# Kernel tuning notes

Hardware: AMD Instinct MI355X
Metric: run time of the kernel (lower is better)

Reference implementation:

```python
import jax, jax.numpy as jnp
import numpy as np
import math

NHEAD = 8
OUT = 64
EF = 64
IN = 256
NTYPES = 5
NH = 50000
NT = 100000
E = 800000
NEG_SLOPE = 0.2

def _uniform(key, shape, fan):
    # matches reset(): uniform(-stdv, stdv), stdv = sqrt(6/(fan_in+fan_out)) over last two dims
    stdv = math.sqrt(6.0 / (shape[-2] + shape[-1]))
    return jax.random.uniform(key, shape, jnp.float32, -stdv, stdv)

def setup_inputs() -> dict:
    key = jax.random.key(0)
    ks = jax.random.split(key, 12)
    head_feature = jax.random.normal(ks[0], (NH, IN), jnp.float32)
    tail_feature = jax.random.normal(ks[1], (NT, IN), jnp.float32)
    head_ind = jax.random.randint(ks[2], (E,), 0, NH)
    tail_ind = jax.random.randint(ks[3], (E,), 0, NT)
    tmp_edge = jax.random.randint(ks[4], (E,), 0, NTYPES)
    edge_emb = _uniform(ks[5], (NTYPES, EF), None)
    W = _uniform(ks[6], (IN, OUT * NHEAD), None)
    W_e = _uniform(ks[7], (EF, EF * NHEAD), None)
    a_l = _uniform(ks[8], (1, NHEAD, OUT), None)
    a_r = _uniform(ks[9], (1, NHEAD, OUT), None)
    a_e = _uniform(ks[10], (1, NHEAD, EF), None)
    return {"head_feature": head_feature, "tail_feature": tail_feature,
            "head_ind": head_ind, "tail_ind": tail_ind, "tmp_edge": tmp_edge,
            "edge_emb": edge_emb, "W": W, "W_e": W_e,
            "a_l": a_l, "a_r": a_r, "a_e": a_e}

def reference(head_feature, tail_feature, head_ind, tail_ind, tmp_edge,
              edge_emb, W, W_e, a_l, a_r, a_e):
    n_head_nodes = head_feature.shape[0]
    # projections (dropout is identity in eval)
    h_head = (head_feature @ W).reshape(-1, NHEAD, OUT)   # [NH, H, D]
    h_tail = (tail_feature @ W).reshape(-1, NHEAD, OUT)   # [NT, H, D]
    e = (edge_emb @ W_e).reshape(-1, NHEAD, EF)           # [T, H, EF]
    # per-edge attention logits, all heads at once: [E, H]
    h_l = jnp.sum(a_l * h_head, axis=-1)[head_ind]
    h_r = jnp.sum(a_r * h_tail, axis=-1)[tail_ind]
    h_e = jnp.sum(a_e * e, axis=-1)[tmp_edge]
    att = jax.nn.leaky_relu(h_l + h_r + h_e, NEG_SLOPE)
    # sparse (per-destination-row) softmax, vectorized over heads
    seg_max = jax.ops.segment_max(att, head_ind, num_segments=n_head_nodes)
    att = jnp.exp(att - seg_max[head_ind])
    denom = jax.ops.segment_sum(att, head_ind, num_segments=n_head_nodes)
    att = att / denom[head_ind]                           # [E, H]
    # weighted aggregation per head (small fixed loop over heads)
    outs = [jax.ops.segment_sum(att[:, n:n + 1] * h_tail[tail_ind, n, :],
                                head_ind, num_segments=n_head_nodes)
            for n in range(NHEAD)]
    out = jnp.stack(outs, axis=1).reshape(n_head_nodes, -1)  # [NH, H*D]
    return out, att
```

## Files before the change

### kernel.cpp

```cpp
#include <hip/hip_runtime.h>

#define NH 50000
#define NT 100000
#define NE 800000
#define MPAD 100096

typedef __attribute__((ext_vector_type(8))) short bf16x8;
typedef __attribute__((ext_vector_type(4))) float f32x4;

__device__ __forceinline__ unsigned short f2bf(float f){
  unsigned int u = __float_as_uint(f);
  u += 0x7FFFu + ((u >> 16) & 1u);
  return (unsigned short)(u >> 16);
}

__device__ __forceinline__ void fma8(float* acc, float w, uint4 pk){
  acc[0] += w*__uint_as_float(pk.x<<16); acc[1] += w*__uint_as_float(pk.x&0xFFFF0000u);
  acc[2] += w*__uint_as_float(pk.y<<16); acc[3] += w*__uint_as_float(pk.y&0xFFFF0000u);
  acc[4] += w*__uint_as_float(pk.z<<16); acc[5] += w*__uint_as_float(pk.z&0xFFFF0000u);
  acc[6] += w*__uint_as_float(pk.w<<16); acc[7] += w*__uint_as_float(pk.w&0xFFFF0000u);
}

__global__ void k_prep(const float* __restrict__ W, const float* __restrict__ W_e,
                       const float* __restrict__ edge_emb,
                       const float* __restrict__ a_l, const float* __restrict__ a_r,
                       const float* __restrict__ a_e,
                       unsigned short* __restrict__ wlr_t,
                       float* __restrict__ h_e){
  __shared__ float s_al[512], s_ar[512], s_ae[512], s_wef[512];
  int t = threadIdx.x;
  for (int i=t;i<512;i+=256){ s_al[i]=a_l[i]; s_ar[i]=a_r[i]; s_ae[i]=a_e[i]; }
  __syncthreads();
  { int k = t;
    for (int h=0;h<8;h++){
      float accl=0.f, accr=0.f;
      for (int d=0; d<64; d++){
        float w = W[k*512 + h*64 + d];
        accl += w*s_al[h*64+d];
        accr += w*s_ar[h*64+d];
      }
      wlr_t[h*256 + k]     = f2bf(accl);
      wlr_t[(8+h)*256 + k] = f2bf(accr);
    }
  }
  if (t<64){
    for (int h=0;h<8;h++){
      float acc=0.f;
      for (int f=0; f<64; f++) acc += W_e[t*512 + h*64 + f]*s_ae[h*64+f];
      s_wef[t*8+h]=acc;
    }
  }
  __syncthreads();
  if (t<40){
    int ty=t>>3, h=t&7;
    float acc=0.f;
    for (int k2=0;k2<64;k2++) acc += edge_emb[ty*64+k2]*s_wef[k2*8+h];
    h_e[t]=acc;
  }
}

__global__ void k_wt(const float* __restrict__ W, unsigned short* __restrict__ Wt){
  int n = blockIdx.x, k = threadIdx.x;
  Wt[n*256+k] = f2bf(W[k*512+n]);
}

__global__ __launch_bounds__(256) void k_hl(const float* __restrict__ head_f,
      const unsigned short* __restrict__ wlr_t, float* __restrict__ h_l){
  __shared__ unsigned short As[256*64];
  __shared__ unsigned short Bs[16*256];
  int t = threadIdx.x;
  int wave = t>>6, lane = t&63;
  int lr = lane&15, lq = lane>>4;
  long r0 = (long)blockIdx.x*256;

#pragma unroll
  for (int i=0;i<2;i++){
    int q = i*256 + t;
    int c = q>>5, un = q&31;
    float4 v = *(const float4*)(wlr_t + c*256 + un*8);
    int u = un ^ (c&7);
    *(float4*)((char*)Bs + c*512 + u*16) = v;
  }

  f32x4 acc[4];
#pragma unroll
  for (int mf=0;mf<4;mf++) acc[mf]=(f32x4){0.f,0.f,0.f,0.f};

  for (int kt=0; kt<4; kt++){
    __syncthreads();
#pragma unroll
    for (int i=0;i<16;i++){
      int q = i*256+t;
      int row = q>>4, cg = q&15;
      long gr = r0 + row;
      float4 v = make_float4(0.f,0.f,0.f,0.f);
      if (gr < NH) v = *(const float4*)(head_f + gr*256 + kt*64 + cg*4);
      int u = (cg>>1) ^ (row&7);
      ushort4 sv;
      sv.x=f2bf(v.x); sv.y=f2bf(v.y); sv.z=f2bf(v.z); sv.w=f2bf(v.w);
      *(ushort4*)((char*)As + row*128 + u*16 + (cg&1)*8) = sv;
    }
    __syncthreads();
#pragma unroll
    for (int ks=0;ks<2;ks++){
      int un = kt*8 + ks*4 + lq;
      int cu = un ^ (lr&7);
      bf16x8 bfr = *(const bf16x8*)((const char*)Bs + lr*512 + cu*16);
#pragma unroll
      for (int mf=0;mf<4;mf++){
        int r = wave*64 + mf*16 + lr;
        int u = (ks*4+lq) ^ (r&7);
        bf16x8 afr = *(const bf16x8*)((const char*)As + r*128 + u*16);
        acc[mf] = __builtin_amdgcn_mfma_f32_16x16x32_bf16(afr, bfr, acc[mf], 0,0,0);
      }
    }
  }
#pragma unroll
  for (int mf=0;mf<4;mf++)
#pragma unroll
    for (int j=0;j<4;j++){
      long grow = r0 + wave*64 + mf*16 + lq*4 + j;
      if (grow < NH && lr < 8) h_l[grow*8+lr] = acc[mf][j];
    }
}

__global__ __launch_bounds__(256) void k_gemm(const float* __restrict__ Aref,
      const unsigned short* __restrict__ Wt, const float* __restrict__ a_r_g,
      unsigned short* __restrict__ Cout, float* __restrict__ h_r){
  __shared__ unsigned short As[128*64];
  __shared__ unsigned short Bs[128*64];
  int t = threadIdx.x;
  int m0 = blockIdx.x*128;
  int n0 = blockIdx.y*128;
  int wave = t>>6, lane = t&63;
  int wm = (wave>>1)*64, wn = (wave&1)*64;
  int lr = lane & 15, lq = lane >> 4;

  f32x4 acc[4][4];
#pragma unroll
  for (int mf=0;mf<4;mf++)
#pragma unroll
    for (int nf=0;nf<4;nf++) acc[mf][nf] = (f32x4){0.f,0.f,0.f,0.f};

  for (int kt=0; kt<4; kt++){
#pragma unroll
    for (int i=0;i<8;i++){
      int q = i*256 + t;
      int row = q>>4;
      int cg  = q&15;
      int grow = m0 + row;
      float4 v = make_float4(0.f,0.f,0.f,0.f);
      if (grow < NT) v = *(const float4*)(Aref + (size_t)grow*256 + kt*64 + cg*4);
      int u  = (cg>>1) ^ (row&7);
      ushort4 sv;
      sv.x=f2bf(v.x); sv.y=f2bf(v.y); sv.z=f2bf(v.z); sv.w=f2bf(v.w);
      *(ushort4*)((char*)As + row*128 + u*16 + (cg&1)*8) = sv;
    }
#pragma unroll
    for (int i=0;i<4;i++){
      int q = i*256 + t;
      int row = q>>3;
      int un  = q&7;
      float4 v = *(const float4*)(Wt + (size_t)(n0+row)*256 + kt*64 + un*8);
      int u = un ^ (row&7);
      *(float4*)((char*)Bs + row*128 + u*16) = v;
    }
    __syncthreads();

    bf16x8 af[2][4], bfr[2][4];
#pragma unroll
    for (int ks=0;ks<2;ks++)
#pragma unroll
      for (int mf=0;mf<4;mf++){
        int r = wm + mf*16 + lr;
        int u = (ks*4 + lq) ^ (r&7);
        af[ks][mf] = *(const bf16x8*)((const char*)As + r*128 + u*16);
      }
#pragma unroll
    for (int ks=0;ks<2;ks++)
#pragma unroll
      for (int nf=0;nf<4;nf++){
        int c = wn + nf*16 + lr;
        int u = (ks*4 + lq) ^ (c&7);
        bfr[ks][nf] = *(const bf16x8*)((const char*)Bs + c*128 + u*16);
      }
#pragma unroll
    for (int ks=0;ks<2;ks++)
#pragma unroll
      for (int mf=0;mf<4;mf++)
#pragma unroll
        for (int nf=0;nf<4;nf++)
          acc[mf][nf] = __builtin_amdgcn_mfma_f32_16x16x32_bf16(af[ks][mf], bfr[ks][nf], acc[mf][nf], 0,0,0);
    __syncthreads();
  }
#pragma unroll
  for (int mf=0;mf<4;mf++)
#pragma unroll
    for (int nf=0;nf<4;nf++){
      int gr = m0 + wm + mf*16 + lq*4;
      int gc = n0 + wn + nf*16 + lr;
#pragma unroll
      for (int j=0;j<4;j++)
        Cout[(size_t)(gr+j)*512 + gc] = f2bf(acc[mf][nf][j]);
    }
  {
    int h = (n0 + wn) >> 6;
    float w[4];
#pragma unroll
    for (int nf=0;nf<4;nf++) w[nf] = a_r_g[h*64 + nf*16 + lr];
#pragma unroll
    for (int mf=0;mf<4;mf++)
#pragma unroll
      for (int j=0;j<4;j++){
        float s = acc[mf][0][j]*w[0] + acc[mf][1][j]*w[1]
                + acc[mf][2][j]*w[2] + acc[mf][3][j]*w[3];
        s += __shfl_xor(s, 1); s += __shfl_xor(s, 2);
        s += __shfl_xor(s, 4); s += __shfl_xor(s, 8);
        int gr = m0 + wm + mf*16 + lq*4 + j;
        if (lr == 0 && gr < NT) h_r[(size_t)gr*8 + h] = s;
      }
  }
}

__global__ void k_hist(const int* __restrict__ head_ind, int* __restrict__ cnt){
  int e = blockIdx.x*256 + threadIdx.x;
  atomicAdd(&cnt[head_ind[e]], 1);
}

__global__ void k_scan1(const int* __restrict__ cnt, int* __restrict__ bsum){
  __shared__ int s[256];
  int b=blockIdx.x, t=threadIdx.x, g=b*256+t;
  s[t] = (g<NH)? cnt[g] : 0;
  __syncthreads();
  for (int off=128; off>0; off>>=1){ if (t<off) s[t]+=s[t+off]; __syncthreads(); }
  if (t==0) bsum[b]=s[0];
}
__global__ void k_scan2(int* __restrict__ bsum, int nb){
  __shared__ int s[256];
  int t=threadIdx.x;
  int v = (t<nb)? bsum[t] : 0;
  s[t]=v; __syncthreads();
  for (int off=1; off<256; off<<=1){
    int u = (t>=off)? s[t-off] : 0; __syncthreads();
    s[t]+=u; __syncthreads();
  }
  if (t<nb) bsum[t] = s[t]-v;
}
__global__ void k_scan3(const int* __restrict__ cnt, const int* __restrict__ bsum,
                        int* __restrict__ offs, int* __restrict__ cur){
  __shared__ int s[256];
  int b=blockIdx.x, t=threadIdx.x, g=b*256+t;
  int v=(g<NH)? cnt[g] : 0;
  s[t]=v; __syncthreads();
  for (int off=1; off<256; off<<=1){
    int u=(t>=off)? s[t-off] : 0; __syncthreads();
    s[t]+=u; __syncthreads();
  }
  int excl = s[t]-v + bsum[b];
  if (g<NH){
    offs[g]=excl; cur[g]=excl;
    if (g==NH-1) offs[NH]=excl+v;
  }
}

__global__ void k_logit2(const int* __restrict__ head_ind, const int* __restrict__ tail_ind,
                         const int* __restrict__ tmp_edge,
                         const float* __restrict__ h_l, const float* __restrict__ h_r,
                         const float* __restrict__ h_e,
                         int* __restrict__ cur,
                         float* __restrict__ att_csr,
                         int* __restrict__ edge_of, int* __restrict__ tail_s){
  int g = blockIdx.x*256 + threadIdx.x;
  int e = g>>3, h = g&7, l = threadIdx.x&63;
  int hd = head_ind[e], tl = tail_ind[e], ty = tmp_edge[e];
  float v = h_l[hd*8+h] + h_r[(size_t)tl*8+h] + h_e[ty*8+h];
  v = v > 0.f ? v : 0.2f*v;
  int p = 0;
  if (h==0) p = atomicAdd(&cur[hd], 1);
  p = __shfl(p, l & ~7);
  att_csr[p*8+h] = v;
  if (h==0){ edge_of[p]=e; tail_s[p]=tl; }
}

__global__ __launch_bounds__(256) void k_agg3(const int* __restrict__ offs,
      const int* __restrict__ edge_of, const int* __restrict__ tail_s,
      const float* __restrict__ att_csr,
      const unsigned short* __restrict__ h_tail,
      float* __restrict__ att, float* __restrict__ out){
  int t = threadIdx.x;
  int l = t & 63;
  int i = blockIdx.x*4 + (t>>6);
  int h = l & 7, hq = l >> 3;
  int s0 = offs[i];
  int deg = offs[i+1] - s0;

  float m = -1e30f;
  for (int q = hq; q < deg; q += 8) m = fmaxf(m, att_csr[(s0+q)*8 + h]);
  m = fmaxf(m, __shfl_xor(m, 8));
  m = fmaxf(m, __shfl_xor(m, 16));
  m = fmaxf(m, __shfl_xor(m, 32));
  float sum = 0.f;
  for (int q = hq; q < deg; q += 8) sum += __expf(att_csr[(s0+q)*8 + h] - m);
  sum += __shfl_xor(sum, 8); sum += __shfl_xor(sum, 16); sum += __shfl_xor(sum, 32);
  float r = (deg > 0) ? 1.f/sum : 0.f;

  float mh = __shfl(m, hq), rh = __shfl(r, hq);
  bool wlane = (l & 7) == 0;
  float acc[8];
#pragma unroll
  for (int c=0;c<8;c++) acc[c]=0.f;
  int j = 0;
  for (; j+4 <= deg; j += 4){
    int p0=s0+j, p1=p0+1, p2=p0+2, p3=p0+3;
    int t0=tail_s[p0], t1=tail_s[p1], t2=tail_s[p2], t3=tail_s[p3];
    float a0=att_csr[p0*8+hq], a1=att_csr[p1*8+hq];
    float a2=att_csr[p2*8+hq], a3=att_csr[p3*8+hq];
    uint4 r0 = *(const uint4*)(h_tail + (size_t)t0*512 + l*8);
    uint4 r1 = *(const uint4*)(h_tail + (size_t)t1*512 + l*8);
    uint4 r2 = *(const uint4*)(h_tail + (size_t)t2*512 + l*8);
    uint4 r3 = *(const uint4*)(h_tail + (size_t)t3*512 + l*8);
    float w0=__expf(a0-mh)*rh, w1=__expf(a1-mh)*rh;
    float w2=__expf(a2-mh)*rh, w3=__expf(a3-mh)*rh;
    if (wlane){
      __builtin_nontemporal_store(w0, &att[(size_t)edge_of[p0]*8 + hq]);
      __builtin_nontemporal_store(w1, &att[(size_t)edge_of[p1]*8 + hq]);
      __builtin_nontemporal_store(w2, &att[(size_t)edge_of[p2]*8 + hq]);
      __builtin_nontemporal_store(w3, &att[(size_t)edge_of[p3]*8 + hq]);
    }
    fma8(acc, w0, r0);
    fma8(acc, w1, r1);
    fma8(acc, w2, r2);
    fma8(acc, w3, r3);
  }
  for (; j < deg; j++){
    int p0 = s0+j;
    int t0 = tail_s[p0];
    float a0 = att_csr[p0*8 + hq];
    uint4 r0 = *(const uint4*)(h_tail + (size_t)t0*512 + l*8);
    float w0 = __expf(a0 - mh) * rh;
    if (wlane) __builtin_nontemporal_store(w0, &att[(size_t)edge_of[p0]*8 + hq]);
    fma8(acc, w0, r0);
  }
  float* o = out + (size_t)i*512 + l*8;
  f32x4 v0 = {acc[0],acc[1],acc[2],acc[3]};
  f32x4 v1 = {acc[4],acc[5],acc[6],acc[7]};
  __builtin_nontemporal_store(v0, (f32x4*)o);
  __builtin_nontemporal_store(v1, (f32x4*)(o+4));
}

extern "C" void kernel_launch(void* const* d_in, const int* in_sizes, int n_in,
                              void* d_out, int out_size, void* d_ws, size_t ws_size,
                              hipStream_t stream) {
  const float* head_f   = (const float*)d_in[0];
  const float* tail_f   = (const float*)d_in[1];
  const int*   head_ind = (const int*)d_in[2];
  const int*   tail_ind = (const int*)d_in[3];
  const int*   tmp_edge = (const int*)d_in[4];
  const float* edge_emb = (const float*)d_in[5];
  const float* W        = (const float*)d_in[6];
  const float* W_e      = (const float*)d_in[7];
  const float* a_l      = (const float*)d_in[8];
  const float* a_r      = (const float*)d_in[9];
  const float* a_e      = (const float*)d_in[10];

  float* out = (float*)d_out;
  float* att = out + (size_t)NH*512;

  char* ws = (char*)d_ws;
  auto alloc = [&](size_t bytes)->char*{ char* p = ws; ws += (bytes+511)&~(size_t)511; return p; };
  unsigned short* Wt    = (unsigned short*)alloc((size_t)512*256*2);
  unsigned short* wlr_t = (unsigned short*)alloc((size_t)16*256*2);
  float* h_e            = (float*)alloc(512);
  float* h_l            = (float*)alloc((size_t)NH*8*4);
  float* h_r            = (float*)alloc((size_t)NT*8*4);
  unsigned short* h_tail= (unsigned short*)alloc((size_t)MPAD*512*2);
  int* cnt              = (int*)alloc((size_t)NH*4);
  int* offs             = (int*)alloc((size_t)(NH+1)*4);
  int* cur              = (int*)alloc((size_t)NH*4);
  int* bsum             = (int*)alloc(1024);
  int* edge_of          = (int*)alloc((size_t)NE*4);
  int* tail_s           = (int*)alloc((size_t)NE*4);
  float* att_csr        = (float*)alloc((size_t)NE*8*4);

  hipMemsetAsync(cnt, 0, (size_t)NH*4, stream);
  k_prep<<<1,256,0,stream>>>(W, W_e, edge_emb, a_l, a_r, a_e, wlr_t, h_e);
  k_wt<<<512,256,0,stream>>>(W, Wt);
  k_hl<<<(NH+255)/256,256,0,stream>>>(head_f, wlr_t, h_l);
  k_gemm<<<dim3(MPAD/128,4),256,0,stream>>>(tail_f, Wt, a_r, h_tail, h_r);
  k_hist<<<NE/256,256,0,stream>>>(head_ind, cnt);
  k_scan1<<<196,256,0,stream>>>(cnt, bsum);
  k_scan2<<<1,256,0,stream>>>(bsum, 196);
  k_scan3<<<196,256,0,stream>>>(cnt, bsum, offs, cur);
  k_logit2<<<NE*8/256,256,0,stream>>>(head_ind, tail_ind, tmp_edge, h_l, h_r, h_e,
                                      cur, att_csr, edge_of, tail_s);
  k_agg3<<<NH/4,256,0,stream>>>(offs, edge_of, tail_s, att_csr, h_tail, att, out);
}
```

Measured before the change: 465.6 us.

## Pre-convert tail features to bf16 and double-buffer GEMM with direct global-to-LDS loads

Adds a separate pass that converts tail_feature to bf16 into the output buffer, used as scratch before it is overwritten. The tail projection GEMM now stages A and B tiles straight into LDS with global_load_lds into two buffers, prefetching the next K tile while computing the current one. It also remaps block IDs so each XCD works on a contiguous range of tiles. The aim is to remove in-loop fp32-to-bf16 conversion and register staging and to overlap loads with MFMA, at the cost of an extra conversion kernel's memory traffic.

```diff
diff --git a/kernel.cpp b/kernel.cpp
--- a/kernel.cpp
+++ b/kernel.cpp
@@ -7,6 +7,7 @@
 
 typedef __attribute__((ext_vector_type(8))) short bf16x8;
 typedef __attribute__((ext_vector_type(4))) float f32x4;
+typedef __attribute__((ext_vector_type(8))) unsigned short u16x8;
 
 __device__ __forceinline__ unsigned short f2bf(float f){
   unsigned int u = __float_as_uint(f);
@@ -19,6 +20,12 @@
   acc[2] += w*__uint_as_float(pk.y<<16); acc[3] += w*__uint_as_float(pk.y&0xFFFF0000u);
   acc[4] += w*__uint_as_float(pk.z<<16); acc[5] += w*__uint_as_float(pk.z&0xFFFF0000u);
   acc[6] += w*__uint_as_float(pk.w<<16); acc[7] += w*__uint_as_float(pk.w&0xFFFF0000u);
+}
+
+__device__ __forceinline__ void gl2lds16(const unsigned short* g, unsigned short* l){
+  __builtin_amdgcn_global_load_lds(
+      (const __attribute__((address_space(1))) void*)g,
+      (__attribute__((address_space(3))) void*)l, 16, 0, 0);
 }
 
 __global__ void k_prep(const float* __restrict__ W, const float* __restrict__ W_e,
@@ -64,6 +71,18 @@
   Wt[n*256+k] = f2bf(W[k*512+n]);
 }
 
+__global__ __launch_bounds__(256) void k_cvt(const float* __restrict__ A,
+                                             unsigned short* __restrict__ Ab){
+  size_t g = (size_t)blockIdx.x*256 + threadIdx.x;
+  const float* src = A + g*8;
+  float4 v0 = *(const float4*)(src);
+  float4 v1 = *(const float4*)(src + 4);
+  u16x8 s;
+  s[0]=f2bf(v0.x); s[1]=f2bf(v0.y); s[2]=f2bf(v0.z); s[3]=f2bf(v0.w);
+  s[4]=f2bf(v1.x); s[5]=f2bf(v1.y); s[6]=f2bf(v1.z); s[7]=f2bf(v1.w);
+  *(u16x8*)(Ab + g*8) = s;
+}
+
 __global__ __launch_bounds__(256) void k_hl(const float* __restrict__ head_f,
       const unsigned short* __restrict__ wlr_t, float* __restrict__ h_l){
   __shared__ unsigned short As[256*64];
@@ -124,17 +143,38 @@
     }
 }
 
-__global__ __launch_bounds__(256) void k_gemm(const float* __restrict__ Aref,
+__global__ __launch_bounds__(256) void k_gemm2(const unsigned short* __restrict__ A_bf,
       const unsigned short* __restrict__ Wt, const float* __restrict__ a_r_g,
       unsigned short* __restrict__ Cout, float* __restrict__ h_r){
-  __shared__ unsigned short As[128*64];
-  __shared__ unsigned short Bs[128*64];
+  __shared__ unsigned short As[2][128*64];
+  __shared__ unsigned short Bs[2][128*64];
   int t = threadIdx.x;
-  int m0 = blockIdx.x*128;
-  int n0 = blockIdx.y*128;
   int wave = t>>6, lane = t&63;
+  int lr = lane & 15, lq = lane >> 4;
+
+  int bid = blockIdx.x;
+  int wg  = (bid & 7)*391 + (bid >> 3);
+  int m0 = (wg >> 2)*128;
+  int n0 = (wg & 3)*128;
+
+  auto STAGE = [&](int buf, int kt){
+#pragma unroll
+    for (int i=0;i<4;i++){
+      int v = wave*256 + i*64 + lane;
+      int row = v>>3, un = (v&7) ^ (row&7);
+      gl2lds16(A_bf + (size_t)(m0+row)*256 + kt*64 + un*8,
+               &As[buf][(wave*256 + i*64)*8]);
+    }
+#pragma unroll
+    for (int i=0;i<4;i++){
+      int v = wave*256 + i*64 + lane;
+      int n = v>>3, un = (v&7) ^ (n&7);
+      gl2lds16(Wt + (size_t)(n0+n)*256 + kt*64 + un*8,
+               &Bs[buf][(wave*256 + i*64)*8]);
+    }
+  };
+
   int wm = (wave>>1)*64, wn = (wave&1)*64;
-  int lr = lane & 15, lq = lane >> 4;
 
   f32x4 acc[4][4];
 #pragma unroll
@@ -142,30 +182,11 @@
 #pragma unroll
     for (int nf=0;nf<4;nf++) acc[mf][nf] = (f32x4){0.f,0.f,0.f,0.f};
 
+  STAGE(0, 0);
+  __syncthreads();
+  int cur = 0;
   for (int kt=0; kt<4; kt++){
-#pragma unroll
-    for (int i=0;i<8;i++){
-      int q = i*256 + t;
-      int row = q>>4;
-      int cg  = q&15;
-      int grow = m0 + row;
-      float4 v = make_float4(0.f,0.f,0.f,0.f);
-      if (grow < NT) v = *(const float4*)(Aref + (size_t)grow*256 + kt*64 + cg*4);
-      int u  = (cg>>1) ^ (row&7);
-      ushort4 sv;
-      sv.x=f2bf(v.x); sv.y=f2bf(v.y); sv.z=f2bf(v.z); sv.w=f2bf(v.w);
-      *(ushort4*)((char*)As + row*128 + u*16 + (cg&1)*8) = sv;
-    }
-#pragma unroll
-    for (int i=0;i<4;i++){
-      int q = i*256 + t;
-      int row = q>>3;
-      int un  = q&7;
-      float4 v = *(const float4*)(Wt + (size_t)(n0+row)*256 + kt*64 + un*8);
-      int u = un ^ (row&7);
-      *(float4*)((char*)Bs + row*128 + u*16) = v;
-    }
-    __syncthreads();
+    if (kt < 3) STAGE(cur^1, kt+1);
 
     bf16x8 af[2][4], bfr[2][4];
 #pragma unroll
@@ -174,7 +195,7 @@
       for (int mf=0;mf<4;mf++){
         int r = wm + mf*16 + lr;
         int u = (ks*4 + lq) ^ (r&7);
-        af[ks][mf] = *(const bf16x8*)((const char*)As + r*128 + u*16);
+        af[ks][mf] = *(const bf16x8*)((const char*)As[cur] + r*128 + u*16);
       }
 #pragma unroll
     for (int ks=0;ks<2;ks++)
@@ -182,7 +203,7 @@
       for (int nf=0;nf<4;nf++){
         int c = wn + nf*16 + lr;
         int u = (ks*4 + lq) ^ (c&7);
-        bfr[ks][nf] = *(const bf16x8*)((const char*)Bs + c*128 + u*16);
+        bfr[ks][nf] = *(const bf16x8*)((const char*)Bs[cur] + c*128 + u*16);
       }
 #pragma unroll
     for (int ks=0;ks<2;ks++)
@@ -192,6 +213,7 @@
         for (int nf=0;nf<4;nf++)
           acc[mf][nf] = __builtin_amdgcn_mfma_f32_16x16x32_bf16(af[ks][mf], bfr[ks][nf], acc[mf][nf], 0,0,0);
     __syncthreads();
+    cur ^= 1;
   }
 #pragma unroll
   for (int mf=0;mf<4;mf++)
@@ -365,6 +387,7 @@
 
   float* out = (float*)d_out;
   float* att = out + (size_t)NH*512;
+  unsigned short* A_bf = (unsigned short*)d_out;
 
   char* ws = (char*)d_ws;
   auto alloc = [&](size_t bytes)->char*{ char* p = ws; ws += (bytes+511)&~(size_t)511; return p; };
@@ -385,8 +408,9 @@
   hipMemsetAsync(cnt, 0, (size_t)NH*4, stream);
   k_prep<<<1,256,0,stream>>>(W, W_e, edge_emb, a_l, a_r, a_e, wlr_t, h_e);
   k_wt<<<512,256,0,stream>>>(W, Wt);
+  k_cvt<<<12500,256,0,stream>>>(tail_f, A_bf);
   k_hl<<<(NH+255)/256,256,0,stream>>>(head_f, wlr_t, h_l);
-  k_gemm<<<dim3(MPAD/128,4),256,0,stream>>>(tail_f, Wt, a_r, h_tail, h_r);
+  k_gemm2<<<3128,256,0,stream>>>(A_bf, Wt, a_r, h_tail, h_r);
   k_hist<<<NE/256,256,0,stream>>>(head_ind, cnt);
   k_scan1<<<196,256,0,stream>>>(cnt, bsum);
   k_scan2<<<1,256,0,stream>>>(bsum, 196);
```

Result: faster. 436.8 us (-6.2%).
